# Optimization experiments

Measured on AMD Instinct MI355X. Metric: run time of the kernel, lower is better.

Reference implementation:

```python
import jax, jax.numpy as jnp
import numpy as np

N1, N2 = 8192, 8192
E1, E2 = 131072, 131072
F_IN, NH, B = 64, 128, 256
D6 = 6 * NH  # set2set in_channels = 768


def _gcn(x, W, b, src, dst, ew, n):
    xw = x @ W
    loop = jnp.arange(n)
    s = jnp.concatenate([src, loop])
    d = jnp.concatenate([dst, loop])
    w = jnp.concatenate([ew, jnp.ones((n,), ew.dtype)])
    deg = jax.ops.segment_sum(w, d, num_segments=n)
    dinv = jnp.where(deg > 0, jax.lax.rsqrt(deg), 0.0)
    norm = (dinv[s] * w * dinv[d])[:, None]
    return jax.ops.segment_sum(xw[s] * norm, d, num_segments=n) + b


def _leaky(x):
    return jax.nn.leaky_relu(x, 0.2)


def _l2norm(x):
    return x / jnp.maximum(jnp.linalg.norm(x, axis=1, keepdims=True), 1e-12)


def _set2set(x, batch, nseg, Wih, Whh, bih, bhh, steps=2):
    # Set2Set pooling: LSTM(input=2d, hidden=d) + segment softmax attention
    d = x.shape[1]
    h = jnp.zeros((nseg, d), x.dtype)
    c = jnp.zeros((nseg, d), x.dtype)
    q_star = jnp.zeros((nseg, 2 * d), x.dtype)
    for _ in range(steps):
        gates = q_star @ Wih.T + h @ Whh.T + bih + bhh
        gi, gf, gg, go = jnp.split(gates, 4, axis=1)  # torch LSTM gate order i,f,g,o
        c = jax.nn.sigmoid(gf) * c + jax.nn.sigmoid(gi) * jnp.tanh(gg)
        h = jax.nn.sigmoid(go) * jnp.tanh(c)
        e = jnp.sum(x * h[batch], axis=1)
        emax = jax.ops.segment_max(e, batch, num_segments=nseg)
        ee = jnp.exp(e - emax[batch])
        a = ee / jax.ops.segment_sum(ee, batch, num_segments=nseg)[batch]
        r = jax.ops.segment_sum(a[:, None] * x, batch, num_segments=nseg)
        q_star = jnp.concatenate([h, r], axis=1)
    return q_star


def setup_inputs():
    key = jax.random.key(0)
    ks = jax.random.split(key, 20)
    f32 = jnp.float32

    def xav(k, shp):
        fan_in, fan_out = shp[-1], shp[0] if len(shp) == 2 else shp[-1]
        lim = float(np.sqrt(6.0 / (shp[0] + shp[1])))
        return jax.random.uniform(k, shp, f32, -lim, lim)

    inp = {}
    inp["features_1"] = jax.random.normal(ks[0], (N1, F_IN), f32)
    inp["features_2"] = jax.random.normal(ks[1], (N2, F_IN), f32)
    inp["edge_attr_1"] = jax.random.uniform(ks[2], (E1,), f32)
    inp["edge_attr_2"] = jax.random.uniform(ks[3], (E2,), f32)
    inp["W0"] = xav(ks[4], (F_IN, NH)); inp["b0"] = jnp.zeros((NH,), f32)
    inp["W1"] = xav(ks[5], (NH, NH)); inp["b1"] = jnp.zeros((NH,), f32)
    inp["W2"] = xav(ks[6], (NH, NH)); inp["b2"] = jnp.zeros((NH,), f32)
    inp["Wih"] = xav(ks[7], (4 * D6, 2 * D6)); inp["bih"] = jnp.zeros((4 * D6,), f32)
    inp["Whh"] = xav(ks[8], (4 * D6, D6)); inp["bhh"] = jnp.zeros((4 * D6,), f32)
    inp["Wp1"] = xav(ks[9], (256, 4 * D6)); inp["bp1"] = jnp.zeros((256,), f32)
    inp["Wp2"] = xav(ks[10], (128, 256)); inp["bp2"] = jnp.zeros((128,), f32)
    inp["Wp3"] = xav(ks[11], (1, 128)); inp["bp3"] = jnp.zeros((1,), f32)
    inp["edge_index_1"] = jax.random.randint(ks[12], (2, E1), 0, N1)
    inp["edge_index_2"] = jax.random.randint(ks[13], (2, E2), 0, N2)
    inp["batch_1"] = jnp.sort(jax.random.randint(ks[14], (N1,), 0, B))
    inp["batch_2"] = jnp.sort(jax.random.randint(ks[15], (N2,), 0, B))
    return inp


def reference(features_1, features_2, edge_attr_1, edge_attr_2,
              W0, b0, W1, b1, W2, b2, Wih, bih, Whh, bhh,
              Wp1, bp1, Wp2, bp2, Wp3, bp3,
              edge_index_1, edge_index_2, batch_1, batch_2):
    s1, d1 = edge_index_1[0], edge_index_1[1]
    s2, d2 = edge_index_2[0], edge_index_2[1]

    f1a = _leaky(_gcn(features_1, W0, b0, s1, d1, edge_attr_1, N1))
    f2a = _leaky(_gcn(features_2, W0, b0, s2, d2, edge_attr_2, N2))
    f1b = _leaky(_gcn(f1a, W1, b1, s1, d1, edge_attr_1, N1))
    f2b = _leaky(_gcn(f2a, W1, b1, s2, d2, edge_attr_2, N2))
    f1c = _leaky(_gcn(f1b, W2, b2, s1, d1, edge_attr_1, N1))
    f2c = _leaky(_gcn(f2b, W2, b2, s2, d2, edge_attr_2, N2))
    h1 = jnp.concatenate([f1a, f1b, f1c], axis=1)  # [N1, 3*NH]
    h2 = jnp.concatenate([f2a, f2b, f2c], axis=1)  # [N2, 3*NH]

    # interaction: cosine-sim map masked to same-graph pairs (len_map)
    ns = _l2norm(h1)
    nv = _l2norm(h2)
    mask = (batch_1[:, None] == batch_2[None, :]).astype(ns.dtype)  # [N1, N2]
    imap = (ns @ nv.T) * mask
    f1 = jnp.concatenate([ns, imap @ nv], axis=1)      # [N1, 6*NH]
    f2 = jnp.concatenate([nv, imap.T @ ns], axis=1)    # [N2, 6*NH]

    g1 = _set2set(f1, batch_1, B, Wih, Whh, bih, bhh)  # [B, 12*NH]
    g2 = _set2set(f2, batch_2, B, Wih, Whh, bih, bhh)  # [B, 12*NH]
    z = jnp.concatenate([g1, g2], axis=1)              # [B, 24*NH]
    z = jax.nn.relu(z @ Wp1.T + bp1)
    z = jax.nn.relu(z @ Wp2.T + bp2)
    z = z @ Wp3.T + bp3
    return jax.nn.sigmoid(z).reshape(-1)
```

## Files before the change

kernel.cpp:

```cpp
#include <hip/hip_runtime.h>
#include <cmath>

#define N_NODES 8192
#define N_EDGES 131072
#define NB      256
#define NH      128
#define D3      384
#define D6      768
#define SMM     96

typedef __attribute__((ext_vector_type(8))) short short8v;
typedef __attribute__((ext_vector_type(4))) float f32x4;
typedef unsigned short bf16t;

__device__ __forceinline__ float sigf(float x){ return 1.0f/(1.0f+__expf(-x)); }
__device__ __forceinline__ unsigned short f2bf(float x){
  unsigned u = __float_as_uint(x);
  unsigned r = u + 0x7FFF + ((u>>16)&1);
  return (unsigned short)(r>>16);
}
__device__ __forceinline__ float bfl(unsigned u){ return __uint_as_float(u<<16); }
__device__ __forceinline__ float bfh(unsigned u){ return __uint_as_float(u & 0xFFFF0000u); }
__device__ __forceinline__ float b2f(bf16t u){ return __uint_as_float(((unsigned)u)<<16); }
__device__ __forceinline__ float h0val(const float* bih, const float* bhh, int j){
  float c = sigf(bih[j]+bhh[j]) * tanhf(bih[2*D6+j]+bhh[2*D6+j]);
  return sigf(bih[3*D6+j]+bhh[3*D6+j]) * tanhf(c);
}


__global__ void k_init(float* deg1, float* deg2, int* ecnt1, int* ecnt2, int* cnt1, int* cnt2){
  int t = blockIdx.x*blockDim.x + threadIdx.x;
  if (t < N_NODES){ deg1[t]=1.f; deg2[t]=1.f; ecnt1[t]=0; ecnt2[t]=0; }
  if (t < NB){ cnt1[t]=0; cnt2[t]=0; }
}

__global__ void k_deg(const int* __restrict__ ei1, const float* __restrict__ ea1, float* deg1, int* ecnt1,
                      const int* __restrict__ ei2, const float* __restrict__ ea2, float* deg2, int* ecnt2,
                      const int* __restrict__ b1, const int* __restrict__ b2, int* cnt1, int* cnt2){
  int idx = blockIdx.x*blockDim.x + threadIdx.x;
  int side = idx >= N_EDGES;
  int e = idx & (N_EDGES-1);
  const int* ei = side? ei2:ei1; const float* ea = side? ea2:ea1;
  float* deg = side? deg2:deg1;  int* ecnt = side? ecnt2:ecnt1;
  int d = ei[N_EDGES+e];
  atomicAdd(&deg[d], ea[e]);
  atomicAdd(&ecnt[d], 1);
  if (idx < N_NODES){ atomicAdd(&cnt1[b1[idx]],1); atomicAdd(&cnt2[b2[idx]],1); }
}

__global__ __launch_bounds__(256) void k_scan256(const int* c1, const int* c2, int* s1, int* s2){
  const int* c = blockIdx.x? c2:c1; int* st = blockIdx.x? s2:s1;
  __shared__ int ps[256];
  int t = threadIdx.x;
  ps[t]=c[t]; __syncthreads();
  for (int d=1; d<256; d<<=1){
    int v = (t>=d)? ps[t-d]:0;
    __syncthreads();
    ps[t]+=v;
    __syncthreads();
  }
  st[t+1]=ps[t];
  if (t==0) st[0]=0;
}

__global__ __launch_bounds__(1024) void k_escan(const int* ec1, const int* ec2,
                                                int* off1, int* cur1, int* off2, int* cur2){
  const int* cnt = blockIdx.x? ec2:ec1;
  int* off = blockIdx.x? off2:off1;
  int* cur = blockIdx.x? cur2:cur1;
  __shared__ int ps[1024];
  int t = threadIdx.x;
  int base = t*8;
  int loc[8]; int s=0;
  #pragma unroll
  for (int k=0;k<8;k++){ loc[k]=s; s+=cnt[base+k]; }
  ps[t]=s; __syncthreads();
  for (int d=1; d<1024; d<<=1){
    int v = (t>=d)? ps[t-d]:0;
    __syncthreads();
    ps[t]+=v;
    __syncthreads();
  }
  int pre = (t==0)? 0 : ps[t-1];
  #pragma unroll
  for (int k=0;k<8;k++){ int v=pre+loc[k]; off[base+k]=v; cur[base+k]=v; }
  if (t==1023) off[N_NODES]=ps[1023];
}

__global__ void k_fill(const int* __restrict__ ei1, const float* __restrict__ ea1, const float* __restrict__ d1,
                       int* cur1, int* es1, float* ec1,
                       const int* __restrict__ ei2, const float* __restrict__ ea2, const float* __restrict__ d2,
                       int* cur2, int* es2, float* ec2){
  int idx = blockIdx.x*blockDim.x + threadIdx.x;
  int side = idx >= N_EDGES;
  int e = idx & (N_EDGES-1);
  const int* ei = side? ei2:ei1; const float* ea = side? ea2:ea1;
  const float* deg = side? d2:d1;
  int* cur = side? cur2:cur1; int* es = side? es2:es1; float* ec = side? ec2:ec1;
  int s = ei[e], d = ei[N_EDGES+e];
  int pos = atomicAdd(&cur[d], 1);
  es[pos] = s;
  ec[pos] = rsqrtf(deg[s])*ea[e]*rsqrtf(deg[d]);
}

__global__ __launch_bounds__(256) void k_szero(uint4* p){
  p[blockIdx.x*256 + threadIdx.x] = make_uint4(0,0,0,0);
}


__global__ __launch_bounds__(128) void k_xw(const float* __restrict__ x1, const float* __restrict__ x2,
                                            int xs, int K, const float* __restrict__ W,
                                            bf16t* __restrict__ xw1, bf16t* __restrict__ xw2){
  __shared__ float xr[8][128];
  int blk = blockIdx.x;
  int side = blk >> 10; int b = blk & 1023;
  const float* x = side? x2:x1;
  bf16t* xw = side? xw2:xw1;
  int i0 = b*8;
  int c = threadIdx.x;
  for (int idx=c; idx<8*K; idx+=128){
    int r = idx / K, k = idx - r*K;
    xr[r][k] = x[(size_t)(i0+r)*xs + k];
  }
  __syncthreads();
  float acc[8]={0,0,0,0,0,0,0,0};
  for (int k=0;k<K;k++){
    float w = W[k*NH+c];
    #pragma unroll
    for (int r=0;r<8;r++) acc[r]+=xr[r][k]*w;
  }
  #pragma unroll
  for (int r=0;r<8;r++) xw[(size_t)(i0+r)*NH+c]=f2bf(acc[r]);
}

__global__ __launch_bounds__(256) void k_gather(const bf16t* __restrict__ xw1, const bf16t* __restrict__ xw2,
                                                const int* __restrict__ off1, const int* __restrict__ off2,
                                                const int* __restrict__ es1, const int* __restrict__ es2,
                                                const float* __restrict__ ec1, const float* __restrict__ ec2,
                                                const float* __restrict__ d1, const float* __restrict__ d2,
                                                const float* __restrict__ b,
                                                float* __restrict__ h1, float* __restrict__ h2, int loff,
                                                int l2mode, bf16t* __restrict__ f1, bf16t* __restrict__ f2){
  int blk = blockIdx.x;
  int side = blk >> 10; int bb = blk & 1023;
  const ushort4* xw = (const ushort4*)(side? xw2:xw1);
  const int* off = side? off2:off1;
  const int* es  = side? es2:es1;
  const float* ec= side? ec2:ec1;
  const float* deg = side? d2:d1;
  float* h = side? h2:h1;
  int t = threadIdx.x;
  int i = bb*8 + (t>>5);
  int c4 = t & 31;
  float sc = 1.0f/deg[i];
  ushort4 v = xw[(size_t)i*32 + c4];
  float4 acc = {b2f(v.x)*sc, b2f(v.y)*sc, b2f(v.z)*sc, b2f(v.w)*sc};
  int r = off[i], r1 = off[i+1];
  for (; r+3<r1; r+=4){
    int s0=es[r], s1=es[r+1], s2=es[r+2], s3=es[r+3];
    float w0=ec[r], w1=ec[r+1], w2=ec[r+2], w3=ec[r+3];
    ushort4 u0 = xw[(size_t)s0*32 + c4];
    ushort4 u1 = xw[(size_t)s1*32 + c4];
    ushort4 u2 = xw[(size_t)s2*32 + c4];
    ushort4 u3 = xw[(size_t)s3*32 + c4];
    acc.x += b2f(u0.x)*w0 + b2f(u1.x)*w1 + b2f(u2.x)*w2 + b2f(u3.x)*w3;
    acc.y += b2f(u0.y)*w0 + b2f(u1.y)*w1 + b2f(u2.y)*w2 + b2f(u3.y)*w3;
    acc.z += b2f(u0.z)*w0 + b2f(u1.z)*w1 + b2f(u2.z)*w2 + b2f(u3.z)*w3;
    acc.w += b2f(u0.w)*w0 + b2f(u1.w)*w1 + b2f(u2.w)*w2 + b2f(u3.w)*w3;
  }
  for (; r<r1; r++){
    int s0=es[r]; float w0=ec[r];
    ushort4 u0 = xw[(size_t)s0*32 + c4];
    acc.x+=b2f(u0.x)*w0; acc.y+=b2f(u0.y)*w0; acc.z+=b2f(u0.z)*w0; acc.w+=b2f(u0.w)*w0;
  }
  float4 bv = ((const float4*)b)[c4];
  acc.x+=bv.x; acc.y+=bv.y; acc.z+=bv.z; acc.w+=bv.w;
  acc.x = (acc.x>0.f)?acc.x:0.2f*acc.x;
  acc.y = (acc.y>0.f)?acc.y:0.2f*acc.y;
  acc.z = (acc.z>0.f)?acc.z:0.2f*acc.z;
  acc.w = (acc.w>0.f)?acc.w:0.2f*acc.w;
  if (!l2mode){
    ((float4*)(h + (size_t)i*D3 + loff))[c4] = acc;
  } else {
    float4 v0 = ((const float4*)(h + (size_t)i*D3))[c4];
    float4 v1 = ((const float4*)(h + (size_t)i*D3 + 128))[c4];
    float ss = v0.x*v0.x+v0.y*v0.y+v0.z*v0.z+v0.w*v0.w
             + v1.x*v1.x+v1.y*v1.y+v1.z*v1.z+v1.w*v1.w
             + acc.x*acc.x+acc.y*acc.y+acc.z*acc.z+acc.w*acc.w;
    #pragma unroll
    for (int m=1;m<32;m<<=1) ss += __shfl_xor(ss, m, 64);
    float scale = 1.0f/fmaxf(sqrtf(ss), 1e-12f);
    bf16t* f = side? f2:f1;
    ((ushort4*)(f + (size_t)i*D6))[c4]       = make_ushort4(f2bf(v0.x*scale),f2bf(v0.y*scale),f2bf(v0.z*scale),f2bf(v0.w*scale));
    ((ushort4*)(f + (size_t)i*D6 + 128))[c4] = make_ushort4(f2bf(v1.x*scale),f2bf(v1.y*scale),f2bf(v1.z*scale),f2bf(v1.w*scale));
    ((ushort4*)(f + (size_t)i*D6 + 256))[c4] = make_ushort4(f2bf(acc.x*scale),f2bf(acc.y*scale),f2bf(acc.z*scale),f2bf(acc.w*scale));
  }
}

__global__ __launch_bounds__(256) void k_smat(const bf16t* __restrict__ f1, const bf16t* __restrict__ f2,
                                              const int* __restrict__ st1, const int* __restrict__ st2,
                                              bf16t* __restrict__ S, bf16t* __restrict__ ST){
  int g = blockIdx.x;
  int it2 = blockIdx.y/3, jt2 = blockIdx.y - it2*3;
  int i0 = st1[g]; int n1 = st1[g+1]-i0; if (n1>SMM) n1=SMM;
  int j0 = st2[g]; int n2 = st2[g+1]-j0; if (n2>SMM) n2=SMM;
  if (it2*32 >= n1 || jt2*32 >= n2) return;
  int w = threadIdx.x >> 6, lane = threadIdx.x & 63;
  int lm = lane & 15, quad = lane >> 4;
  int ti = it2*2 + (w>>1), tj = jt2*2 + (w&1);
  if (ti*16 >= n1 || tj*16 >= n2) return;
  const bf16t* a = f1 + (size_t)(i0 + ti*16 + lm)*D6 + quad*8;
  const bf16t* b = f2 + (size_t)(j0 + tj*16 + lm)*D6 + quad*8;
  f32x4 acc = {0,0,0,0};
  #pragma unroll
  for (int k=0; k<384; k+=32){
    short8v af = *(const short8v*)(a + k);
    short8v bf = *(const short8v*)(b + k);
    acc = __builtin_amdgcn_mfma_f32_16x16x32_bf16(af, bf, acc, 0, 0, 0);
  }
  bf16t* Sg  = S  + (size_t)g*SMM*SMM;
  bf16t* STg = ST + (size_t)g*SMM*SMM;
  int col = tj*16 + lm;
  #pragma unroll
  for (int r=0;r<4;r++){
    int row = ti*16 + quad*4 + r;
    if (row < n1 && col < n2){
      bf16t v = f2bf(acc[r]);
      Sg [(size_t)row*SMM + col] = v;
      STg[(size_t)col*SMM + row] = v;
    }
  }
}

__global__ __launch_bounds__(256) void k_apply(bf16t* __restrict__ f1, bf16t* __restrict__ f2,
                                               const int* __restrict__ st1, const int* __restrict__ st2,
                                               const bf16t* __restrict__ S, const bf16t* __restrict__ ST){
  __shared__ bf16t tbuf[32*392];
  int bx = blockIdx.x;
  int side = bx >> 8, g = bx & (NB-1);
  int a0 = st1[g]; int n1 = st1[g+1]-a0; if (n1>SMM) n1=SMM;
  int b0 = st2[g]; int n2 = st2[g+1]-b0; if (n2>SMM) n2=SMM;
  int cnt = side? n2 : n1;
  int J   = side? n1 : n2;
  int r0 = blockIdx.y*32;
  if (r0 >= cnt) return;
  const bf16t* src = side? (f1 + (size_t)a0*D6) : (f2 + (size_t)b0*D6);
  bf16t* dst = (side? (f2 + (size_t)b0*D6) : (f1 + (size_t)a0*D6)) + D3;
  const bf16t* Sg = (side? ST : S) + (size_t)g*SMM*SMM;
  int t = threadIdx.x, w = t>>6, lane = t&63;
  int lm = lane & 15, quad = lane >> 4;
  int mt1 = (cnt - r0 > 16) ? 2 : 1;
  f32x4 acc[2][6] = {};
  for (int kb = 0; kb < J; kb += 32){
    __syncthreads();
    for (int idx = t; idx < 32*48; idx += 256){
      int j = idx/48, cg = idx - j*48;
      uint4 v = (kb+j < J)? ((const uint4*)(src + (size_t)(kb+j)*D6))[cg] : make_uint4(0,0,0,0);
      *(uint4*)(tbuf + j*392 + cg*8) = v;
    }
    short8v af0, af1;
    {
      const bf16t* ap = Sg + (size_t)(r0 + lm)*SMM + kb + quad*8;
      af0 = *(const short8v*)ap;
      af1 = (mt1 > 1)? *(const short8v*)(ap + 16*SMM) : af0;
    }
    __syncthreads();
    #pragma unroll
    for (int ni = 0; ni < 6; ni++){
      int nt = w*6 + ni;
      short8v bf;
      #pragma unroll
      for (int ji = 0; ji < 8; ji++)
        bf[ji] = (short)tbuf[(quad*8 + ji)*392 + nt*16 + lm];
      acc[0][ni] = __builtin_amdgcn_mfma_f32_16x16x32_bf16(af0, bf, acc[0][ni], 0, 0, 0);
      if (mt1 > 1)
        acc[1][ni] = __builtin_amdgcn_mfma_f32_16x16x32_bf16(af1, bf, acc[1][ni], 0, 0, 0);
    }
  }
  for (int mt = 0; mt < mt1; mt++)
    for (int ni = 0; ni < 6; ni++){
      int nt = w*6 + ni;
      #pragma unroll
      for (int r = 0; r < 4; r++){
        int row = r0 + mt*16 + quad*4 + r;
        if (row < cnt) dst[(size_t)row*D6 + nt*16 + lm] = f2bf(acc[mt][ni][r]);
      }
    }
}


__global__ __launch_bounds__(64) void k_cvec(const float* __restrict__ Wih, const float* __restrict__ Whh,
                                             const float* __restrict__ bih, const float* __restrict__ bhh,
                                             float* __restrict__ cvec){
  __shared__ float hs[D6];
  int j = blockIdx.x, lane = threadIdx.x;
  for (int k=lane; k<D6; k+=64) hs[k] = h0val(bih,bhh,k);
  __syncthreads();
  const float4* wi = (const float4*)(Wih + (size_t)j*(2*D6));
  const float4* wh = (const float4*)(Whh + (size_t)j*D6);
  const float4* h4 = (const float4*)hs;
  float acc=0;
  #pragma unroll
  for (int m=0;m<3;m++){
    float4 hv = h4[m*64+lane];
    float4 a = wi[m*64+lane];
    float4 b = wh[m*64+lane];
    acc += hv.x*(a.x+b.x) + hv.y*(a.y+b.y) + hv.z*(a.z+b.z) + hv.w*(a.w+b.w);
  }
  #pragma unroll
  for (int m=1;m<64;m<<=1) acc += __shfl_xor(acc,m,64);
  if (lane==0) cvec[j]=acc+bih[j]+bhh[j];
}

__global__ __launch_bounds__(256) void k_att(const bf16t* __restrict__ f1, const bf16t* __restrict__ f2,
                                             const float* __restrict__ hbase, int perseg,
                                             const float* __restrict__ bih, const float* __restrict__ bhh,
                                             const int* __restrict__ st1, const int* __restrict__ st2,
                                             bf16t* __restrict__ dst16, long sidestep, long dstride){
  __shared__ float4 hs[192];
  __shared__ float e_s[SMM];
  __shared__ float part[4][D6];
  int side = blockIdx.x >> 8, g = blockIdx.x & (NB-1);
  const int* st = side? st2:st1;
  int n0 = st[g]; int cnt = st[g+1]-n0; if (cnt>SMM) cnt=SMM;
  const bf16t* x = (side? f2:f1) + (size_t)n0*D6;
  int t = threadIdx.x, w = t>>6, lane = t&63;
  if (t<192){
    if (perseg){
      hs[t] = ((const float4*)(hbase + (size_t)(side*NB+g)*D6))[t];
    } else {
      int j = t*4;
      hs[t] = make_float4(h0val(bih,bhh,j), h0val(bih,bhh,j+1), h0val(bih,bhh,j+2), h0val(bih,bhh,j+3));
    }
  }
  __syncthreads();
  for (int n=w; n<cnt; n+=4){
    const uint2* xr = (const uint2*)(x + (size_t)n*D6);
    float p = 0;
    #pragma unroll
    for (int m=0;m<3;m++){
      uint2 rv = xr[m*64+lane];
      float4 hvv = hs[m*64+lane];
      p += bfl(rv.x)*hvv.x + bfh(rv.x)*hvv.y + bfl(rv.y)*hvv.z + bfh(rv.y)*hvv.w;
    }
    #pragma unroll
    for (int m=1;m<64;m<<=1) p += __shfl_xor(p,m,64);
    if (lane==0) e_s[n]=p;
  }
  __syncthreads();
  if (w==0){
    float mx=-INFINITY;
    for (int n=lane;n<cnt;n+=64) mx=fmaxf(mx,e_s[n]);
    #pragma unroll
    for (int m=1;m<64;m<<=1) mx=fmaxf(mx,__shfl_xor(mx,m,64));
    float s=0;
    for (int n=lane;n<cnt;n+=64) s+=__expf(e_s[n]-mx);
    #pragma unroll
    for (int m=1;m<64;m<<=1) s+=__shfl_xor(s,m,64);
    float inv=1.0f/s;
    for (int n=lane;n<cnt;n+=64) e_s[n]=__expf(e_s[n]-mx)*inv;
  }
  __syncthreads();
  float av[3][4] = {};
  for (int n=w; n<cnt; n+=4){
    float a = e_s[n];
    const uint2* xr = (const uint2*)(x + (size_t)n*D6);
    #pragma unroll
    for (int m=0;m<3;m++){
      uint2 rv = xr[m*64+lane];
      av[m][0]+=a*bfl(rv.x); av[m][1]+=a*bfh(rv.x); av[m][2]+=a*bfl(rv.y); av[m][3]+=a*bfh(rv.y);
    }
  }
  #pragma unroll
  for (int m=0;m<3;m++)
    *(float4*)&part[w][(m*64+lane)*4] = make_float4(av[m][0],av[m][1],av[m][2],av[m][3]);
  __syncthreads();
  if (t<192){
    float4 p0 = *(const float4*)&part[0][t*4];
    float4 p1 = *(const float4*)&part[1][t*4];
    float4 p2 = *(const float4*)&part[2][t*4];
    float4 p3 = *(const float4*)&part[3][t*4];
    float4 s = make_float4(p0.x+p1.x+p2.x+p3.x, p0.y+p1.y+p2.y+p3.y,
                           p0.z+p1.z+p2.z+p3.z, p0.w+p1.w+p2.w+p3.w);
    ushort4 o = make_ushort4(f2bf(s.x), f2bf(s.y), f2bf(s.z), f2bf(s.w));
    ((ushort4*)(dst16 + side*sidestep + (size_t)g*dstride))[t]=o;
  }
}

__global__ __launch_bounds__(256) void k_gemm_mfma(const short* __restrict__ A16,
                                                   const short* __restrict__ B16,
                                                   float* __restrict__ pout){
  int w = threadIdx.x >> 6, lane = threadIdx.x & 63;
  int lm = lane & 15, quad = lane >> 4;
  int bm = blockIdx.x * 16;
  int bn = blockIdx.y * 256 + w * 64;
  const short* a = A16 + (size_t)(bm + lm)*768 + quad*8;
  const short* b = B16 + (size_t)(bn + lm)*768 + quad*8;
  f32x4 acc0={0,0,0,0}, acc1={0,0,0,0}, acc2={0,0,0,0}, acc3={0,0,0,0};
  for (int k=0; k<768; k+=32){
    short8v af = *(const short8v*)(a + k);
    short8v b0 = *(const short8v*)(b + k);
    short8v b1 = *(const short8v*)(b + 16*768 + k);
    short8v b2 = *(const short8v*)(b + 32*768 + k);
    short8v b3 = *(const short8v*)(b + 48*768 + k);
    acc0 = __builtin_amdgcn_mfma_f32_16x16x32_bf16(af, b0, acc0, 0, 0, 0);
    acc1 = __builtin_amdgcn_mfma_f32_16x16x32_bf16(af, b1, acc1, 0, 0, 0);
    acc2 = __builtin_amdgcn_mfma_f32_16x16x32_bf16(af, b2, acc2, 0, 0, 0);
    acc3 = __builtin_amdgcn_mfma_f32_16x16x32_bf16(af, b3, acc3, 0, 0, 0);
  }
  #pragma unroll
  for (int r=0;r<4;r++){
    size_t base = (size_t)(bm + quad*4 + r)*3072 + bn + lm;
    pout[base]      = acc0[r];
    pout[base + 16] = acc1[r];
    pout[base + 32] = acc2[r];
    pout[base + 48] = acc3[r];
  }
}

__global__ __launch_bounds__(256) void k_gemm_mfma_p1(const short* __restrict__ A16,
                                                      const short* __restrict__ B16,
                                                      float* __restrict__ pout){
  int w = threadIdx.x >> 6, lane = threadIdx.x & 63;
  int lm = lane & 15, quad = lane >> 4;
  int bm = blockIdx.x * 16;
  int bn = w * 64;
  int kbase = blockIdx.y * 192;
  const short* a = A16 + (size_t)(bm + lm)*3072 + quad*8 + kbase;
  const short* b = B16 + (size_t)(bn + lm)*3072 + quad*8 + kbase;
  f32x4 acc0={0,0,0,0}, acc1={0,0,0,0}, acc2={0,0,0,0}, acc3={0,0,0,0};
  for (int k=0; k<192; k+=32){
    short8v af = *(const short8v*)(a + k);
    short8v b0 = *(const short8v*)(b + k);
    short8v b1 = *(const short8v*)(b + 16*3072 + k);
    short8v b2 = *(const short8v*)(b + 32*3072 + k);
    short8v b3 = *(const short8v*)(b + 48*3072 + k);
    acc0 = __builtin_amdgcn_mfma_f32_16x16x32_bf16(af, b0, acc0, 0, 0, 0);
    acc1 = __builtin_amdgcn_mfma_f32_16x16x32_bf16(af, b1, acc1, 0, 0, 0);
    acc2 = __builtin_amdgcn_mfma_f32_16x16x32_bf16(af, b2, acc2, 0, 0, 0);
    acc3 = __builtin_amdgcn_mfma_f32_16x16x32_bf16(af, b3, acc3, 0, 0, 0);
  }
  float* po = pout + (size_t)blockIdx.y*256*256;
  #pragma unroll
  for (int r=0;r<4;r++){
    size_t base = (size_t)(bm + quad*4 + r)*256 + bn + lm;
    po[base]      = acc0[r];
    po[base + 16] = acc1[r];
    po[base + 32] = acc2[r];
    po[base + 48] = acc3[r];
  }
}

__global__ __launch_bounds__(256) void k_conv_w(const float* __restrict__ W, short* __restrict__ dst){
  int t = blockIdx.x*256 + threadIdx.x;
  int n = t/192, q = t - n*192;
  float4 v = ((const float4*)(W + (size_t)n*1536 + 768))[q];
  short4 o = { (short)f2bf(v.x), (short)f2bf(v.y), (short)f2bf(v.z), (short)f2bf(v.w) };
  ((short4*)dst)[t] = o;
}

__global__ __launch_bounds__(256) void k_conv(const float* __restrict__ src, short* __restrict__ dst){
  int t = blockIdx.x*256 + threadIdx.x;
  float4 v = ((const float4*)src)[t];
  short4 o = { (short)f2bf(v.x), (short)f2bf(v.y), (short)f2bf(v.z), (short)f2bf(v.w) };
  ((short4*)dst)[t] = o;
}

__global__ __launch_bounds__(256) void k_lstm_red(const float* __restrict__ pbuf,
                                                  const float* __restrict__ cvec,
                                                  const float* __restrict__ bih, const float* __restrict__ bhh,
                                                  float* __restrict__ h1s, bf16t* __restrict__ z16){
  int t = blockIdx.x*256 + threadIdx.x;
  int m = t/D6, j = t - m*D6;
  const float* p0 = pbuf + (size_t)m*3072 + j;
  float g4[4];
  #pragma unroll
  for (int q=0;q<4;q++) g4[q] = cvec[q*D6 + j] + p0[q*D6];
  float c0j = sigf(bih[j]+bhh[j]) * tanhf(bih[2*D6+j]+bhh[2*D6+j]);
  float c = sigf(g4[1])*c0j + sigf(g4[0])*tanhf(g4[2]);
  float h = sigf(g4[3])*tanhf(c);
  h1s[(size_t)m*D6 + j] = h;
  int side = m>>8, g = m&255;
  z16[(size_t)g*3072 + side*1536 + j] = f2bf(h);
}

__global__ __launch_bounds__(128) void k_p23(const float* __restrict__ pbuf, const float* __restrict__ bp1,
                                             const float* __restrict__ Wp2, const float* __restrict__ bp2,
                                             const float* __restrict__ Wp3, const float* __restrict__ bp3,
                                             float* __restrict__ out){
  __shared__ float zr[256];
  __shared__ float ws[2];
  int m = blockIdx.x, t = threadIdx.x;
  float2 zacc = ((const float2*)(bp1))[t];
  #pragma unroll
  for (int p=0;p<16;p++){
    float2 v = ((const float2*)(pbuf + (size_t)p*256*256 + (size_t)m*256))[t];
    zacc.x += v.x; zacc.y += v.y;
  }
  zr[2*t]   = fmaxf(zacc.x, 0.f);
  zr[2*t+1] = fmaxf(zacc.y, 0.f);
  __syncthreads();
  const float4* wrow = (const float4*)(Wp2 + (size_t)t*256);
  const float4* z4 = (const float4*)zr;
  float acc = bp2[t];
  #pragma unroll 8
  for (int k=0;k<64;k++){
    float4 wv = wrow[k], zv = z4[k];
    acc += wv.x*zv.x + wv.y*zv.y + wv.z*zv.z + wv.w*zv.w;
  }
  float p = fmaxf(acc,0.f)*Wp3[t];
  #pragma unroll
  for (int o=32;o;o>>=1) p += __shfl_down(p,o,64);
  if ((t&63)==0) ws[t>>6]=p;
  __syncthreads();
  if (t==0){ float v=ws[0]+ws[1]+bp3[0]; out[m]=1.0f/(1.0f+__expf(-v)); }
}


extern "C" void kernel_launch(void* const* d_in, const int* in_sizes, int n_in,
                              void* d_out, int out_size, void* d_ws, size_t ws_size,
                              hipStream_t stream){
  const float* feat1=(const float*)d_in[0];
  const float* feat2=(const float*)d_in[1];
  const float* ea1  =(const float*)d_in[2];
  const float* ea2  =(const float*)d_in[3];
  const float* W0=(const float*)d_in[4];  const float* b0=(const float*)d_in[5];
  const float* W1=(const float*)d_in[6];  const float* b1=(const float*)d_in[7];
  const float* W2=(const float*)d_in[8];  const float* b2=(const float*)d_in[9];
  const float* Wih=(const float*)d_in[10]; const float* bih=(const float*)d_in[11];
  const float* Whh=(const float*)d_in[12]; const float* bhh=(const float*)d_in[13];
  const float* Wp1=(const float*)d_in[14]; const float* bp1=(const float*)d_in[15];
  const float* Wp2=(const float*)d_in[16]; const float* bp2=(const float*)d_in[17];
  const float* Wp3=(const float*)d_in[18]; const float* bp3=(const float*)d_in[19];
  const int* ei1=(const int*)d_in[20]; const int* ei2=(const int*)d_in[21];
  const int* batch1=(const int*)d_in[22]; const int* batch2=(const int*)d_in[23];
  float* out = (float*)d_out;

  float* base = (float*)d_ws;
  size_t off = 0;
  auto alloc = [&](size_t n)->float* { float* r = base + off; off += (n + 255) & ~(size_t)255; return r; };
  float* deg1 = alloc(N_NODES);          float* deg2 = alloc(N_NODES);
  bf16t* xw1  = (bf16t*)alloc((size_t)N_NODES*NH/2);
  bf16t* xw2  = (bf16t*)alloc((size_t)N_NODES*NH/2);
  float* h1   = alloc((size_t)N_NODES*D3);
  float* h2   = alloc((size_t)N_NODES*D3);
  bf16t* f1   = (bf16t*)alloc((size_t)N_NODES*D6/2);
  bf16t* f2   = (bf16t*)alloc((size_t)N_NODES*D6/2);
  float* ecoef1 = alloc(N_EDGES);        float* ecoef2 = alloc(N_EDGES);
  float* cvec = alloc(4*D6);
  bf16t* Sbuf = (bf16t*)alloc((size_t)NB*SMM*SMM);
  bf16t* STbuf= Sbuf + (size_t)NB*SMM*SMM;
  float* h1s  = alloc((size_t)512*D6);
  bf16t* zbuf16 = (bf16t*)alloc((size_t)256*3072/2);
  float* pbuf = alloc((size_t)4*512*3072);
  short* Abuf16 = (short*)alloc((size_t)512*D6/2);
  short* Wih16  = (short*)alloc((size_t)3072*D6/2);
  short* Wp116  = (short*)alloc((size_t)256*3072/2);
  int* cnt1 = (int*)alloc(NB);   int* cnt2 = (int*)alloc(NB);
  int* st1  = (int*)alloc(NB+1); int* st2  = (int*)alloc(NB+1);
  int* ecnt1= (int*)alloc(N_NODES); int* ecnt2 = (int*)alloc(N_NODES);
  int* eoff1= (int*)alloc(N_NODES+1); int* eoff2 = (int*)alloc(N_NODES+1);
  int* ecur1= (int*)alloc(N_NODES); int* ecur2 = (int*)alloc(N_NODES);
  int* esrc1= (int*)alloc(N_EDGES); int* esrc2 = (int*)alloc(N_EDGES);
  (void)ws_size; (void)in_sizes; (void)n_in; (void)out_size;

  k_init   <<<32,256,0,stream>>>(deg1,deg2,ecnt1,ecnt2,cnt1,cnt2);
  k_deg    <<<1024,256,0,stream>>>(ei1,ea1,deg1,ecnt1, ei2,ea2,deg2,ecnt2, batch1,batch2,cnt1,cnt2);
  k_scan256<<<2,256,0,stream>>>(cnt1,cnt2,st1,st2);
  k_escan  <<<2,1024,0,stream>>>(ecnt1,ecnt2,eoff1,ecur1,eoff2,ecur2);
  k_fill   <<<1024,256,0,stream>>>(ei1,ea1,deg1,ecur1,esrc1,ecoef1, ei2,ea2,deg2,ecur2,esrc2,ecoef2);
  k_conv_w <<<2304,256,0,stream>>>(Wih, Wih16);
  k_conv   <<<768,256,0,stream>>>(Wp1, Wp116);
  k_szero  <<<2304,256,0,stream>>>((uint4*)Sbuf);

  const float* Ws[3]={W0,W1,W2}; const float* bs[3]={b0,b1,b2};
  for (int l=0;l<3;l++){
    const float* x1 = (l==0)? feat1 : (h1 + (l-1)*NH);
    const float* x2 = (l==0)? feat2 : (h2 + (l-1)*NH);
    int xs = (l==0)? 64 : D3;
    int K  = (l==0)? 64 : NH;
    k_xw    <<<2048,128,0,stream>>>(x1,x2,xs,K,Ws[l],xw1,xw2);
    k_gather<<<2048,256,0,stream>>>(xw1,xw2,eoff1,eoff2,esrc1,esrc2,ecoef1,ecoef2,
                                    deg1,deg2,bs[l],h1,h2,l*NH,(l==2)?1:0,f1,f2);
  }

  k_smat  <<<dim3(256,9),256,0,stream>>>(f1,f2,st1,st2,Sbuf,STbuf);
  k_apply <<<dim3(512,3),256,0,stream>>>(f1,f2,st1,st2,Sbuf,STbuf);

  k_cvec<<<3072,64,0,stream>>>(Wih,Whh,bih,bhh,cvec);

  k_att<<<512,256,0,stream>>>(f1,f2,(const float*)nullptr,0,bih,bhh,st1,st2,
                              (bf16t*)Abuf16,(long)256*D6,(long)D6);

  k_gemm_mfma<<<dim3(32,12),256,0,stream>>>(Abuf16, Wih16, pbuf);
  k_lstm_red <<<1536,256,0,stream>>>(pbuf,cvec,bih,bhh,h1s,zbuf16);

  k_att<<<512,256,0,stream>>>(f1,f2,h1s,1,bih,bhh,st1,st2,
                              zbuf16+768,(long)1536,(long)3072);

  k_gemm_mfma_p1<<<dim3(16,16),256,0,stream>>>((const short*)zbuf16, Wp116, pbuf);
  k_p23 <<<256,128,0,stream>>>(pbuf, bp1, Wp2, bp2, Wp3, bp3, out);
}
```

Measured before the change: 389.0 us.

## Compute GCN feature transforms with bf16 MFMA and store hidden layers as bf16

Replaces the scalar fp32 X·W kernel with an MFMA 16x16x32 bf16 kernel. It adds two prep kernels: one converts the input features to bf16 and one writes transposed bf16 weights. The per-layer hidden buffers h1/h2 move from fp32 to bf16, which halves the traffic the gather kernel writes and reads and feeds the MFMA path directly. In exchange the layer inputs lose precision and two extra small launches run.

```diff
diff --git a/kernel.cpp b/kernel.cpp
--- a/kernel.cpp
+++ b/kernel.cpp
@@ -107,30 +107,56 @@
   p[blockIdx.x*256 + threadIdx.x] = make_uint4(0,0,0,0);
 }
 
-
-__global__ __launch_bounds__(128) void k_xw(const float* __restrict__ x1, const float* __restrict__ x2,
-                                            int xs, int K, const float* __restrict__ W,
-                                            bf16t* __restrict__ xw1, bf16t* __restrict__ xw2){
-  __shared__ float xr[8][128];
+__global__ __launch_bounds__(256) void k_conv2(const float* __restrict__ a, const float* __restrict__ b,
+                                               short* __restrict__ da, short* __restrict__ db){
+  int t = blockIdx.x*256 + threadIdx.x;
+  int side = t >= 131072; int i = t & 131071;
+  float4 v = ((const float4*)(side? b:a))[i];
+  short4 o = { (short)f2bf(v.x), (short)f2bf(v.y), (short)f2bf(v.z), (short)f2bf(v.w) };
+  ((short4*)(side? db:da))[i] = o;
+}
+
+__global__ __launch_bounds__(256) void k_wt(const float* __restrict__ W0, const float* __restrict__ W1,
+                                            const float* __restrict__ W2, bf16t* __restrict__ Wt){
+  int l = blockIdx.x;
+  const float* W = (l==0)? W0 : ((l==1)? W1 : W2);
+  int K = (l==0)? 64 : 128;
+  bf16t* dst = Wt + ((l==0)? 0 : ((l==1)? 128*64 : 128*64+128*128));
+  for (int idx = threadIdx.x; idx < 128*K; idx += 256){
+    int n = idx / K, k = idx - n*K;
+    dst[idx] = f2bf(W[k*NH + n]);
+  }
+}
+
+
+__global__ __launch_bounds__(256) void k_xw_mfma(const bf16t* __restrict__ x1, const bf16t* __restrict__ x2,
+                                                 int xs, int K, const bf16t* __restrict__ Wt,
+                                                 bf16t* __restrict__ xw1, bf16t* __restrict__ xw2){
   int blk = blockIdx.x;
-  int side = blk >> 10; int b = blk & 1023;
-  const float* x = side? x2:x1;
+  int side = blk >> 8; int b = blk & 255;
+  const bf16t* x = side? x2:x1;
   bf16t* xw = side? xw2:xw1;
-  int i0 = b*8;
-  int c = threadIdx.x;
-  for (int idx=c; idx<8*K; idx+=128){
-    int r = idx / K, k = idx - r*K;
-    xr[r][k] = x[(size_t)(i0+r)*xs + k];
-  }
-  __syncthreads();
-  float acc[8]={0,0,0,0,0,0,0,0};
-  for (int k=0;k<K;k++){
-    float w = W[k*NH+c];
-    #pragma unroll
-    for (int r=0;r<8;r++) acc[r]+=xr[r][k]*w;
-  }
-  #pragma unroll
-  for (int r=0;r<8;r++) xw[(size_t)(i0+r)*NH+c]=f2bf(acc[r]);
+  int w = threadIdx.x>>6, lane = threadIdx.x&63;
+  int lm = lane&15, quad = lane>>4;
+  int r0 = b*32 + (w>>1)*16;
+  int c0 = (w&1)*64;
+  const bf16t* a = x + (size_t)(r0+lm)*xs + quad*8;
+  f32x4 acc[4] = {};
+  for (int k=0;k<K;k+=32){
+    short8v af = *(const short8v*)(a + k);
+    #pragma unroll
+    for (int ni=0;ni<4;ni++){
+      short8v bf = *(const short8v*)(Wt + (size_t)(c0+ni*16+lm)*K + quad*8 + k);
+      acc[ni] = __builtin_amdgcn_mfma_f32_16x16x32_bf16(af, bf, acc[ni], 0,0,0);
+    }
+  }
+  #pragma unroll
+  for (int ni=0;ni<4;ni++)
+    #pragma unroll
+    for (int r=0;r<4;r++){
+      int row = r0 + quad*4 + r, col = c0 + ni*16 + lm;
+      xw[(size_t)row*NH + col] = f2bf(acc[ni][r]);
+    }
 }
 
 __global__ __launch_bounds__(256) void k_gather(const bf16t* __restrict__ xw1, const bf16t* __restrict__ xw2,
@@ -139,7 +165,7 @@
                                                 const float* __restrict__ ec1, const float* __restrict__ ec2,
                                                 const float* __restrict__ d1, const float* __restrict__ d2,
                                                 const float* __restrict__ b,
-                                                float* __restrict__ h1, float* __restrict__ h2, int loff,
+                                                bf16t* __restrict__ h1, bf16t* __restrict__ h2, int loff,
                                                 int l2mode, bf16t* __restrict__ f1, bf16t* __restrict__ f2){
   int blk = blockIdx.x;
   int side = blk >> 10; int bb = blk & 1023;
@@ -148,7 +174,7 @@
   const int* es  = side? es2:es1;
   const float* ec= side? ec2:ec1;
   const float* deg = side? d2:d1;
-  float* h = side? h2:h1;
+  bf16t* h = side? h2:h1;
   int t = threadIdx.x;
   int i = bb*8 + (t>>5);
   int c4 = t & 31;
@@ -180,10 +206,13 @@
   acc.z = (acc.z>0.f)?acc.z:0.2f*acc.z;
   acc.w = (acc.w>0.f)?acc.w:0.2f*acc.w;
   if (!l2mode){
-    ((float4*)(h + (size_t)i*D3 + loff))[c4] = acc;
+    ((ushort4*)(h + (size_t)i*D3 + loff))[c4] =
+      make_ushort4(f2bf(acc.x), f2bf(acc.y), f2bf(acc.z), f2bf(acc.w));
   } else {
-    float4 v0 = ((const float4*)(h + (size_t)i*D3))[c4];
-    float4 v1 = ((const float4*)(h + (size_t)i*D3 + 128))[c4];
+    ushort4 u0 = ((const ushort4*)(h + (size_t)i*D3))[c4];
+    ushort4 u1 = ((const ushort4*)(h + (size_t)i*D3 + 128))[c4];
+    float4 v0 = {b2f(u0.x), b2f(u0.y), b2f(u0.z), b2f(u0.w)};
+    float4 v1 = {b2f(u1.x), b2f(u1.y), b2f(u1.z), b2f(u1.w)};
     float ss = v0.x*v0.x+v0.y*v0.y+v0.z*v0.z+v0.w*v0.w
              + v1.x*v1.x+v1.y*v1.y+v1.z*v1.z+v1.w*v1.w
              + acc.x*acc.x+acc.y*acc.y+acc.z*acc.z+acc.w*acc.w;
@@ -542,8 +571,11 @@
   float* deg1 = alloc(N_NODES);          float* deg2 = alloc(N_NODES);
   bf16t* xw1  = (bf16t*)alloc((size_t)N_NODES*NH/2);
   bf16t* xw2  = (bf16t*)alloc((size_t)N_NODES*NH/2);
-  float* h1   = alloc((size_t)N_NODES*D3);
-  float* h2   = alloc((size_t)N_NODES*D3);
+  bf16t* hb1  = (bf16t*)alloc((size_t)N_NODES*D3/2);
+  bf16t* hb2  = (bf16t*)alloc((size_t)N_NODES*D3/2);
+  bf16t* xf1  = (bf16t*)alloc((size_t)N_NODES*64/2);
+  bf16t* xf2  = (bf16t*)alloc((size_t)N_NODES*64/2);
+  bf16t* Wtb  = (bf16t*)alloc((size_t)(128*64 + 2*128*128)/2);
   bf16t* f1   = (bf16t*)alloc((size_t)N_NODES*D6/2);
   bf16t* f2   = (bf16t*)alloc((size_t)N_NODES*D6/2);
   float* ecoef1 = alloc(N_EDGES);        float* ecoef2 = alloc(N_EDGES);
@@ -571,17 +603,20 @@
   k_fill   <<<1024,256,0,stream>>>(ei1,ea1,deg1,ecur1,esrc1,ecoef1, ei2,ea2,deg2,ecur2,esrc2,ecoef2);
   k_conv_w <<<2304,256,0,stream>>>(Wih, Wih16);
   k_conv   <<<768,256,0,stream>>>(Wp1, Wp116);
+  k_conv2  <<<1024,256,0,stream>>>(feat1, feat2, (short*)xf1, (short*)xf2);
+  k_wt     <<<3,256,0,stream>>>(W0, W1, W2, Wtb);
   k_szero  <<<2304,256,0,stream>>>((uint4*)Sbuf);
 
-  const float* Ws[3]={W0,W1,W2}; const float* bs[3]={b0,b1,b2};
+  const float* bs[3]={b0,b1,b2};
+  const bf16t* Wts[3]={Wtb, Wtb+128*64, Wtb+128*64+128*128};
   for (int l=0;l<3;l++){
-    const float* x1 = (l==0)? feat1 : (h1 + (l-1)*NH);
-    const float* x2 = (l==0)? feat2 : (h2 + (l-1)*NH);
+    const bf16t* x1 = (l==0)? xf1 : (hb1 + (l-1)*NH);
+    const bf16t* x2 = (l==0)? xf2 : (hb2 + (l-1)*NH);
     int xs = (l==0)? 64 : D3;
     int K  = (l==0)? 64 : NH;
-    k_xw    <<<2048,128,0,stream>>>(x1,x2,xs,K,Ws[l],xw1,xw2);
-    k_gather<<<2048,256,0,stream>>>(xw1,xw2,eoff1,eoff2,esrc1,esrc2,ecoef1,ecoef2,
-                                    deg1,deg2,bs[l],h1,h2,l*NH,(l==2)?1:0,f1,f2);
+    k_xw_mfma<<<512,256,0,stream>>>(x1,x2,xs,K,Wts[l],xw1,xw2);
+    k_gather <<<2048,256,0,stream>>>(xw1,xw2,eoff1,eoff2,esrc1,esrc2,ecoef1,ecoef2,
+                                     deg1,deg2,bs[l],hb1,hb2,l*NH,(l==2)?1:0,f1,f2);
   }
 
   k_smat  <<<dim3(256,9),256,0,stream>>>(f1,f2,st1,st2,Sbuf,STbuf);
```

Measured after the change: 375.0 us. 1.04x faster.
